# Kernel tuning notes

Measured on AMD Instinct MI355X. Metric: run time of the kernel, lower is better.

The kernel has to match this reference:

```python
import jax, jax.numpy as jnp
import numpy as np

NUM_HEADS = 16
D_MODEL = 2048
HEAD_DIM = 128
ROPE_BASE = 10000


def setup_inputs() -> dict:
    key = jax.random.key(0)
    k1, k2, k3 = jax.random.split(key, 3)
    B, S = 2, 2048
    x = jax.random.normal(k1, (B, S, D_MODEL), dtype=jnp.float32)
    attn_mask = jnp.ones((B, S), dtype=jnp.int32)
    in_proj = 0.02 * jax.random.normal(k2, (3, D_MODEL, NUM_HEADS, HEAD_DIM), dtype=jnp.float32)
    out_proj = 0.02 * jax.random.normal(k3, (NUM_HEADS, HEAD_DIM, D_MODEL), dtype=jnp.float32)
    return {"x": x, "attn_mask": attn_mask, "in_proj": in_proj, "out_proj": out_proj}


def _rope(t, seq_len):
    # t: [B, S, H, hd]; faithful to RotaryEmbedding.__call__ (concat layout, not interleaved)
    half = HEAD_DIM // 2
    inv_freq = 1.0 / (ROPE_BASE ** (2 * jnp.arange(0, half, dtype=jnp.float32) / HEAD_DIM))
    positions = jnp.arange(seq_len, dtype=jnp.float32)
    angles = positions[:, None] * inv_freq[None, :]            # [S, hd/2]
    cos = jnp.cos(angles)[None, :, None, :]                    # [1, S, 1, hd/2]
    sin = jnp.sin(angles)[None, :, None, :]
    tr = t.reshape(*t.shape[:-1], half, 2)                     # [B,S,H,hd/2,2]
    t0, t1 = tr[..., 0], tr[..., 1]
    out = jnp.concatenate([t0 * cos - t1 * sin, t0 * sin + t1 * cos], axis=-1)
    return out.reshape(t.shape)


def reference(x, attn_mask, in_proj, out_proj):
    B, S, D = x.shape
    qkv = jnp.einsum('bsd,tdhm->tbshm', x, in_proj)            # fused QKV
    q, k, v = qkv[0], qkv[1], qkv[2]
    q = _rope(q, S)
    k = _rope(k, S)
    q = jnp.einsum('bshd->bhsd', q)
    k = jnp.einsum('bshd->bhsd', k)
    v = jnp.einsum('bshd->bhsd', v)
    scores = jnp.einsum('bhqd,bhkd->bhqk', q, k) / jnp.sqrt(jnp.float32(HEAD_DIM))
    # causal mask * key padding mask, with diagonal forced to 1
    causal = jnp.tril(jnp.ones((S, S), dtype=scores.dtype))    # [S,S]
    key_mask = attn_mask.astype(scores.dtype)[:, None, :]      # [B,1,S]
    combined = causal[None, :, :] * key_mask                   # [B,S,S]
    eye = jnp.eye(S, dtype=bool)
    combined = jnp.where(eye[None, :, :], jnp.asarray(1.0, scores.dtype), combined)
    scores = scores + (-(1.0 - combined) * 1e9)[:, None, :, :]  # broadcast over heads
    attn_weights = jax.nn.softmax(scores, axis=-1)
    return jnp.einsum('bhqk,bhkd,hdo->bqo', attn_weights, v, out_proj)
```

## Files before the change

### kernel.cpp

```cpp
#include <hip/hip_runtime.h>
#include <hip/hip_bf16.h>

#define B_   2
#define S_   2048
#define H_   16
#define HD_  128
#define D_   2048
#define BS_  4096
#define SCALE_ 0.08838834764831845f

typedef __hip_bfloat16 bf16;
typedef float f32x4 __attribute__((ext_vector_type(4)));
typedef __bf16 bf16x8 __attribute__((ext_vector_type(8)));
typedef unsigned short u16x8 __attribute__((ext_vector_type(8)));
typedef unsigned short u16x4 __attribute__((ext_vector_type(4)));

static __device__ __forceinline__ unsigned short f2bf_u(float f) {
  bf16 h = __float2bfloat16(f);
  return __builtin_bit_cast(unsigned short, h);
}
static __device__ __forceinline__ void load_lds16(const void* g, void* l) {
  __builtin_amdgcn_global_load_lds((const __attribute__((address_space(1))) void*)g,
                                   (__attribute__((address_space(3))) void*)l, 16, 0, 0);
}

__global__ __launch_bounds__(256) void k_convert(const float* __restrict__ src,
                                                 bf16* __restrict__ dst) {
  const size_t i = ((size_t)blockIdx.x * 256 + threadIdx.x) * 8;
  const float4 a = *(const float4*)(src + i);
  const float4 b = *(const float4*)(src + i + 4);
  u16x8 o;
  o[0] = f2bf_u(a.x); o[1] = f2bf_u(a.y); o[2] = f2bf_u(a.z); o[3] = f2bf_u(a.w);
  o[4] = f2bf_u(b.x); o[5] = f2bf_u(b.y); o[6] = f2bf_u(b.z); o[7] = f2bf_u(b.w);
  *(u16x8*)(dst + i) = o;
}

__global__ __launch_bounds__(256) void k_transpose(const float* __restrict__ src0,
                                                   bf16* __restrict__ dst0) {
  const int z = blockIdx.z;
  const float* src = src0 + (size_t)z * D_ * D_;
  bf16* dst = dst0 + (size_t)z * D_ * D_;
  __shared__ float tile[64][65];
  const int t = threadIdx.x;
  const int x0 = blockIdx.x * 64, y0 = blockIdx.y * 64;
#pragma unroll
  for (int i = 0; i < 16; ++i) {
    int idx = t + i * 256, r = idx >> 6, c = idx & 63;
    tile[r][c] = src[(size_t)(y0 + r) * D_ + x0 + c];
  }
  __syncthreads();
#pragma unroll
  for (int i = 0; i < 16; ++i) {
    int idx = t + i * 256, c = idx >> 6, r = idx & 63;
    dst[(size_t)(x0 + c) * D_ + y0 + r] = __float2bfloat16(tile[r][c]);
  }
}

__global__ __launch_bounds__(256) void k_rope_tables(float* __restrict__ cost,
                                                     float* __restrict__ sint) {
  const int idx = blockIdx.x * 256 + threadIdx.x;
  const int s = idx >> 6, d = idx & 63;
  const float inv = expf(-(float)d * (9.210340371976184f / 64.f));
  const float ang = (float)s * inv;
  cost[idx] = cosf(ang);
  sint[idx] = sinf(ang);
}

template <int MODE>
__global__ __launch_bounds__(512, 4) void k_gemm_p(const bf16* __restrict__ A,
                                                   const bf16* __restrict__ Bt,
                                                   float* __restrict__ Cf,
                                                   bf16* __restrict__ qb,
                                                   bf16* __restrict__ kb,
                                                   bf16* __restrict__ vt,
                                                   const float* __restrict__ cost,
                                                   const float* __restrict__ sint) {
  extern __shared__ __align__(16) char smem[];
  const int tid = threadIdx.x;
  const int w = tid >> 6, lane = tid & 63;
  const int wm = w >> 2, wn = w & 3;
  const int lr = lane & 15, lg = lane >> 4;
  const int brow = blockIdx.x * 128, bcol = blockIdx.y * 256;

  f32x4 acc[4][4] = {};

  auto stage = [&](int kt, int buf) {
    char* base = smem + buf * 24576;
    {
      const int row = tid >> 2, su = tid & 3;
      const int up = su ^ ((row >> 1) & 3);
      load_lds16(A + (size_t)(brow + row) * D_ + kt * 32 + up * 8, base + w * 1024);
    }
#pragma unroll
    for (int i = 0; i < 2; ++i) {
      const int slot = i * 512 + tid;
      const int row = slot >> 2, su = slot & 3;
      const int up = su ^ ((row >> 1) & 3);
      load_lds16(Bt + (size_t)(bcol + row) * D_ + kt * 32 + up * 8,
                 base + 8192 + i * 8192 + w * 1024);
    }
  };

  const int NKT = D_ / 32;
  stage(0, 0); stage(1, 1);
  int bs = 0;
  for (int kt = 0; kt < NKT; ++kt) {
    if (kt < NKT - 1) asm volatile("s_waitcnt vmcnt(3)" ::: "memory");
    else              asm volatile("s_waitcnt vmcnt(0)" ::: "memory");
    __builtin_amdgcn_s_barrier();
    __builtin_amdgcn_sched_barrier(0);
    if (kt + 2 < NKT) {
      int sb = bs + 2; if (sb >= 3) sb -= 3;
      stage(kt + 2, sb);
    }

    const char* base = smem + bs * 24576;
    bf16x8 af[4], bf4[4];
#pragma unroll
    for (int q = 0; q < 4; ++q) {
      const int r = wm * 64 + q * 16 + lr;
      af[q] = *(const bf16x8*)(base + r * 64 + ((lg ^ ((r >> 1) & 3)) * 16));
    }
#pragma unroll
    for (int nf = 0; nf < 4; ++nf) {
      const int r = wn * 64 + nf * 16 + lr;
      bf4[nf] = *(const bf16x8*)(base + 8192 + r * 64 + ((lg ^ ((r >> 1) & 3)) * 16));
    }
    __builtin_amdgcn_s_setprio(1);
#pragma unroll
    for (int q = 0; q < 4; ++q)
#pragma unroll
      for (int nf = 0; nf < 4; ++nf)
        acc[q][nf] = __builtin_amdgcn_mfma_f32_16x16x32_bf16(af[q], bf4[nf], acc[q][nf], 0, 0, 0);
    __builtin_amdgcn_s_setprio(0);
    bs = (bs == 2) ? 0 : bs + 1;
  }

  if (MODE == 1) {
#pragma unroll
    for (int mf = 0; mf < 4; ++mf)
#pragma unroll
      for (int nf = 0; nf < 4; ++nf) {
        const int col = bcol + wn * 64 + nf * 16 + lr;
#pragma unroll
        for (int j = 0; j < 4; ++j) {
          const int row = brow + wm * 64 + mf * 16 + lg * 4 + j;
          Cf[(size_t)row * D_ + col] = acc[mf][nf][j];
        }
      }
  } else {
    const int t = bcol >> 11;
#pragma unroll
    for (int mf = 0; mf < 4; ++mf)
#pragma unroll
      for (int nf = 0; nf < 4; ++nf) {
        const int col = bcol + wn * 64 + nf * 16 + lr;
        const int h = (col >> 7) & (H_ - 1), mm = col & (HD_ - 1);
        if (t == 2) {
          const int row0 = brow + wm * 64 + mf * 16 + lg * 4;
          const int b = row0 >> 11, s0 = row0 & (S_ - 1);
          u16x4 pk;
#pragma unroll
          for (int j = 0; j < 4; ++j) pk[j] = f2bf_u(acc[mf][nf][j]);
          *(u16x4*)(vt + ((size_t)(b * H_ + h) * HD_ + mm) * S_ + s0) = pk;
        } else {
          const int i2 = mm >> 1;
          const bool odd = mm & 1;
#pragma unroll
          for (int j = 0; j < 4; ++j) {
            const int row = brow + wm * 64 + mf * 16 + lg * 4 + j;
            const int b = row >> 11, s = row & (S_ - 1);
            const float val = acc[mf][nf][j];
            const float part = __shfl_xor(val, 1, 64);
            const float c = cost[s * 64 + i2];
            const float sn = sint[s * 64 + i2];
            float o = odd ? (part * sn + val * c) : (val * c - part * sn);
            if (t == 0) o *= SCALE_;
            const int om = odd ? (64 + i2) : i2;
            bf16* dst = (t == 1) ? kb : qb;
            dst[((size_t)(b * H_ + h) * S_ + s) * HD_ + om] = __float2bfloat16(o);
          }
        }
      }
  }
}

__global__ __launch_bounds__(256, 2) void k_attn(const bf16* __restrict__ qb,
                                                 const bf16* __restrict__ kb,
                                                 const bf16* __restrict__ vt,
                                                 const int* __restrict__ mask,
                                                 bf16* __restrict__ attn_b) {
  const int tid = threadIdx.x, w = tid >> 6, lane = tid & 63;
  const int lr = lane & 15, lg = lane >> 4;
  const int qt = (blockIdx.y < 16) ? ((int)gridDim.x - 1 - (int)blockIdx.x)
                                   : (int)blockIdx.x;
  const int q0 = qt * 128;
  const int bh = blockIdx.y;
  const int b = bh >> 4, h = bh & (H_ - 1);
  const bf16* qp = qb + (size_t)bh * S_ * HD_;
  const bf16* kp = kb + (size_t)bh * S_ * HD_;
  const bf16* vp = vt + (size_t)bh * HD_ * S_;
  __shared__ __align__(16) bf16 Ks[2][64 * 128];
  __shared__ __align__(16) bf16 Vs[2][128 * 64];
  __shared__ __align__(16) bf16 Ps[4][16][80];

  const int qrowA = q0 + w * 16 + lr;
  bf16x8 qfA[4], qfB[4];
#pragma unroll
  for (int ks = 0; ks < 4; ++ks) {
    qfA[ks] = *(const bf16x8*)(qp + (size_t)qrowA * HD_ + ks * 32 + lg * 8);
    qfB[ks] = *(const bf16x8*)(qp + (size_t)(qrowA + 64) * HD_ + ks * 32 + lg * 8);
  }

  float mA[4], lA[4], mB[4], lB[4];
  f32x4 oA[8], oB[8];
#pragma unroll
  for (int j = 0; j < 4; ++j) { mA[j] = -INFINITY; lA[j] = 0.f; mB[j] = -INFINITY; lB[j] = 0.f; }
#pragma unroll
  for (int c = 0; c < 8; ++c) { oA[c] = (f32x4)(0.f); oB[c] = (f32x4)(0.f); }

  auto stage = [&](int buf, int k0) {
#pragma unroll
    for (int i = 0; i < 4; ++i) {
      const int slot = i * 256 + tid;
      const int row = slot >> 4, j16 = slot & 15;
      load_lds16(kp + (size_t)(k0 + row) * HD_ + ((j16 ^ (row & 7)) * 8),
                 (char*)&Ks[buf][0] + i * 4096 + w * 1024);
    }
#pragma unroll
    for (int i = 0; i < 4; ++i) {
      const int slot = i * 256 + tid;
      const int row = slot >> 3, j8 = slot & 7;
      load_lds16(vp + (size_t)row * S_ + k0 + ((j8 ^ (row & 7)) * 8),
                 (char*)&Vs[buf][0] + i * 4096 + w * 1024);
    }
  };

  auto sm_pv = [&](f32x4 (&sacc)[4], float (&m_run)[4], float (&l_run)[4],
                   f32x4 (&oacc)[8], const int rbase, const int k0,
                   const int (&mk4)[4], const bf16* vsb) {
    float mblk[4] = {-INFINITY, -INFINITY, -INFINITY, -INFINITY};
#pragma unroll
    for (int n = 0; n < 4; ++n) {
      const int kcol = k0 + n * 16 + lr;
#pragma unroll
      for (int j = 0; j < 4; ++j) {
        const int r = rbase + lg * 4 + j;
        float sv = sacc[n][j];
        const bool allowed = (kcol <= r) && (mk4[n] != 0 || kcol == r);
        sv = allowed ? sv : -1e9f;
        sacc[n][j] = sv;
        mblk[j] = fmaxf(mblk[j], sv);
      }
    }
#pragma unroll
    for (int xm = 1; xm < 16; xm <<= 1)
#pragma unroll
      for (int j = 0; j < 4; ++j)
        mblk[j] = fmaxf(mblk[j], __shfl_xor(mblk[j], xm, 64));

    bool grow = false;
#pragma unroll
    for (int j = 0; j < 4; ++j) grow = grow || (mblk[j] > m_run[j] + 8.f);
    if (__any(grow)) {
      float alpha[4];
#pragma unroll
      for (int j = 0; j < 4; ++j) {
        const float mn = fmaxf(m_run[j], mblk[j]);
        alpha[j] = __expf(m_run[j] - mn);
        m_run[j] = mn;
        l_run[j] *= alpha[j];
      }
#pragma unroll
      for (int c = 0; c < 8; ++c)
#pragma unroll
        for (int j = 0; j < 4; ++j) oacc[c][j] *= alpha[j];
    }

    float psum[4] = {0.f, 0.f, 0.f, 0.f};
#pragma unroll
    for (int n = 0; n < 4; ++n)
#pragma unroll
      for (int j = 0; j < 4; ++j) {
        const float p = __expf(sacc[n][j] - m_run[j]);
        psum[j] += p;
        sacc[n][j] = p;
      }
#pragma unroll
    for (int xm = 1; xm < 16; xm <<= 1)
#pragma unroll
      for (int j = 0; j < 4; ++j)
        psum[j] += __shfl_xor(psum[j], xm, 64);
#pragma unroll
    for (int j = 0; j < 4; ++j) l_run[j] += psum[j];

#pragma unroll
    for (int n = 0; n < 4; ++n)
#pragma unroll
      for (int j = 0; j < 4; ++j)
        Ps[w][lg * 4 + j][n * 16 + lr] = __float2bfloat16(sacc[n][j]);

    bf16x8 pa[2];
#pragma unroll
    for (int ks = 0; ks < 2; ++ks)
      pa[ks] = *(const bf16x8*)(&Ps[w][lr][ks * 32 + lg * 8]);
    __builtin_amdgcn_s_setprio(1);
#pragma unroll
    for (int c = 0; c < 8; ++c) {
#pragma unroll
      for (int ks = 0; ks < 2; ++ks) {
        const int vrow = c * 16 + lr;
        const int unit = (ks * 4 + lg) ^ (vrow & 7);
        const bf16x8 vf = *(const bf16x8*)(vsb + vrow * 64 + unit * 8);
        oacc[c] = __builtin_amdgcn_mfma_f32_16x16x32_bf16(pa[ks], vf, oacc[c], 0, 0, 0);
      }
    }
    __builtin_amdgcn_s_setprio(0);
  };

  const int nt = 2 * qt + 2;
  stage(0, 0);
  asm volatile("s_waitcnt vmcnt(0)" ::: "memory");
  __syncthreads();

  int cur = 0;
  for (int it = 0; it < nt; ++it) {
    const int k0 = it * 64;
    if (it + 1 < nt) stage(cur ^ 1, k0 + 64);

    int mk4[4];
#pragma unroll
    for (int n = 0; n < 4; ++n) mk4[n] = mask[b * S_ + k0 + n * 16 + lr];

    const bf16* ksb = &Ks[cur][0];
    const bf16* vsb = &Vs[cur][0];

    f32x4 sA[4] = {}, sB[4] = {};
    __builtin_amdgcn_s_setprio(1);
#pragma unroll
    for (int n = 0; n < 4; ++n) {
      const int krow = n * 16 + lr;
#pragma unroll
      for (int ks = 0; ks < 4; ++ks) {
        const int j16 = (ks * 4 + lg) ^ (krow & 7);
        const bf16x8 kf = *(const bf16x8*)(ksb + krow * 128 + j16 * 8);
        sA[n] = __builtin_amdgcn_mfma_f32_16x16x32_bf16(qfA[ks], kf, sA[n], 0, 0, 0);
        sB[n] = __builtin_amdgcn_mfma_f32_16x16x32_bf16(qfB[ks], kf, sB[n], 0, 0, 0);
      }
    }
    __builtin_amdgcn_s_setprio(0);

    sm_pv(sA, mA, lA, oA, q0 + w * 16, k0, mk4, vsb);
    sm_pv(sB, mB, lB, oB, q0 + 64 + w * 16, k0, mk4, vsb);

    asm volatile("s_waitcnt vmcnt(0)" ::: "memory");
    __syncthreads();
    cur ^= 1;
  }

#pragma unroll
  for (int j = 0; j < 4; ++j) {
    const float invA = 1.f / lA[j];
    const float invB = 1.f / lB[j];
    const int rA = q0 + w * 16 + lg * 4 + j;
#pragma unroll
    for (int c = 0; c < 8; ++c) {
      attn_b[(size_t)(b * S_ + rA) * D_ + h * HD_ + c * 16 + lr] =
          __float2bfloat16(oA[c][j] * invA);
      attn_b[(size_t)(b * S_ + rA + 64) * D_ + h * HD_ + c * 16 + lr] =
          __float2bfloat16(oB[c][j] * invB);
    }
  }
}

extern "C" void kernel_launch(void* const* d_in, const int* in_sizes, int n_in,
                              void* d_out, int out_size, void* d_ws, size_t ws_size,
                              hipStream_t stream) {
  (void)in_sizes; (void)n_in; (void)out_size; (void)ws_size;
  const float* x        = (const float*)d_in[0];
  const int*   attn_mask= (const int*)d_in[1];
  const float* in_proj  = (const float*)d_in[2];
  const float* out_proj = (const float*)d_in[3];
  float* out = (float*)d_out;
  char* ws = (char*)d_ws;

  bf16*  xb    = (bf16*)(ws + 0);
  bf16*  wqkvT = (bf16*)(ws + 16777216);
  bf16*  woT   = (bf16*)(ws + 41943040);
  float* cost  = (float*)(ws + 50331648);
  float* sint  = (float*)(ws + 50855936);
  bf16*  vt    = (bf16*)(ws + 51380224);
  bf16* qb = (bf16*)d_out;
  bf16* kb = (bf16*)((char*)d_out + 16777216);
  bf16* attn_b = xb;

  static int lds_ok = 0;
  if (!lds_ok) {
    (void)hipFuncSetAttribute((const void*)k_gemm_p<0>,
                              hipFuncAttributeMaxDynamicSharedMemorySize, 73728);
    (void)hipFuncSetAttribute((const void*)k_gemm_p<1>,
                              hipFuncAttributeMaxDynamicSharedMemorySize, 73728);
    lds_ok = 1;
  }

  k_convert<<<4096, 256, 0, stream>>>(x, xb);
  k_transpose<<<dim3(32, 32, 3), 256, 0, stream>>>(in_proj, wqkvT);
  k_transpose<<<dim3(32, 32, 1), 256, 0, stream>>>(out_proj, woT);
  k_rope_tables<<<512, 256, 0, stream>>>(cost, sint);
  k_gemm_p<0><<<dim3(32, 24), 512, 73728, stream>>>(xb, wqkvT, nullptr, qb, kb, vt, cost, sint);
  k_attn<<<dim3(16, 32), 256, 0, stream>>>(qb, kb, vt, attn_mask, attn_b);
  k_gemm_p<1><<<dim3(32, 8), 512, 73728, stream>>>(attn_b, woT, out, nullptr, nullptr, nullptr,
                                                   nullptr, nullptr);
}
```

Before: 302.5 us.

## Read V fragments from global memory, share them across row halves, skip masked last tile

```diff
diff --git a/kernel.cpp b/kernel.cpp
--- a/kernel.cpp
+++ b/kernel.cpp
@@ -201,8 +201,7 @@
   const bf16* kp = kb + (size_t)bh * S_ * HD_;
   const bf16* vp = vt + (size_t)bh * HD_ * S_;
   __shared__ __align__(16) bf16 Ks[2][64 * 128];
-  __shared__ __align__(16) bf16 Vs[2][128 * 64];
-  __shared__ __align__(16) bf16 Ps[4][16][80];
+  __shared__ __align__(16) bf16 Ps[4][2][16][80];
 
   const int qrowA = q0 + w * 16 + lr;
   bf16x8 qfA[4], qfB[4];
@@ -219,7 +218,7 @@
 #pragma unroll
   for (int c = 0; c < 8; ++c) { oA[c] = (f32x4)(0.f); oB[c] = (f32x4)(0.f); }
 
-  auto stage = [&](int buf, int k0) {
+  auto stageK = [&](int buf, int k0) {
 #pragma unroll
     for (int i = 0; i < 4; ++i) {
       const int slot = i * 256 + tid;
@@ -227,18 +226,11 @@
       load_lds16(kp + (size_t)(k0 + row) * HD_ + ((j16 ^ (row & 7)) * 8),
                  (char*)&Ks[buf][0] + i * 4096 + w * 1024);
     }
-#pragma unroll
-    for (int i = 0; i < 4; ++i) {
-      const int slot = i * 256 + tid;
-      const int row = slot >> 3, j8 = slot & 7;
-      load_lds16(vp + (size_t)row * S_ + k0 + ((j8 ^ (row & 7)) * 8),
-                 (char*)&Vs[buf][0] + i * 4096 + w * 1024);
-    }
   };
 
-  auto sm_pv = [&](f32x4 (&sacc)[4], float (&m_run)[4], float (&l_run)[4],
-                   f32x4 (&oacc)[8], const int rbase, const int k0,
-                   const int (&mk4)[4], const bf16* vsb) {
+  auto softmax_g = [&](f32x4 (&sacc)[4], float (&m_run)[4], float (&l_run)[4],
+                       f32x4 (&oacc)[8], const int rbase, const int k0,
+                       const int (&mk4)[4], const int g, bf16x8 (&pa)[2]) {
     float mblk[4] = {-INFINITY, -INFINITY, -INFINITY, -INFINITY};
 #pragma unroll
     for (int n = 0; n < 4; ++n) {
@@ -298,42 +290,28 @@
     for (int n = 0; n < 4; ++n)
 #pragma unroll
       for (int j = 0; j < 4; ++j)
-        Ps[w][lg * 4 + j][n * 16 + lr] = __float2bfloat16(sacc[n][j]);
-
-    bf16x8 pa[2];
+        Ps[w][g][lg * 4 + j][n * 16 + lr] = __float2bfloat16(sacc[n][j]);
 #pragma unroll
     for (int ks = 0; ks < 2; ++ks)
-      pa[ks] = *(const bf16x8*)(&Ps[w][lr][ks * 32 + lg * 8]);
-    __builtin_amdgcn_s_setprio(1);
-#pragma unroll
-    for (int c = 0; c < 8; ++c) {
-#pragma unroll
-      for (int ks = 0; ks < 2; ++ks) {
-        const int vrow = c * 16 + lr;
-        const int unit = (ks * 4 + lg) ^ (vrow & 7);
-        const bf16x8 vf = *(const bf16x8*)(vsb + vrow * 64 + unit * 8);
-        oacc[c] = __builtin_amdgcn_mfma_f32_16x16x32_bf16(pa[ks], vf, oacc[c], 0, 0, 0);
-      }
-    }
-    __builtin_amdgcn_s_setprio(0);
+      pa[ks] = *(const bf16x8*)(&Ps[w][g][lr][ks * 32 + lg * 8]);
   };
 
   const int nt = 2 * qt + 2;
-  stage(0, 0);
+  stageK(0, 0);
   asm volatile("s_waitcnt vmcnt(0)" ::: "memory");
   __syncthreads();
 
   int cur = 0;
   for (int it = 0; it < nt; ++it) {
     const int k0 = it * 64;
-    if (it + 1 < nt) stage(cur ^ 1, k0 + 64);
+    const bool doA = (it + 1 < nt);
+    if (it + 1 < nt) stageK(cur ^ 1, k0 + 64);
 
     int mk4[4];
 #pragma unroll
     for (int n = 0; n < 4; ++n) mk4[n] = mask[b * S_ + k0 + n * 16 + lr];
 
     const bf16* ksb = &Ks[cur][0];
-    const bf16* vsb = &Vs[cur][0];
 
     f32x4 sA[4] = {}, sB[4] = {};
     __builtin_amdgcn_s_setprio(1);
@@ -344,14 +322,27 @@
       for (int ks = 0; ks < 4; ++ks) {
         const int j16 = (ks * 4 + lg) ^ (krow & 7);
         const bf16x8 kf = *(const bf16x8*)(ksb + krow * 128 + j16 * 8);
-        sA[n] = __builtin_amdgcn_mfma_f32_16x16x32_bf16(qfA[ks], kf, sA[n], 0, 0, 0);
+        if (doA) sA[n] = __builtin_amdgcn_mfma_f32_16x16x32_bf16(qfA[ks], kf, sA[n], 0, 0, 0);
         sB[n] = __builtin_amdgcn_mfma_f32_16x16x32_bf16(qfB[ks], kf, sB[n], 0, 0, 0);
       }
     }
     __builtin_amdgcn_s_setprio(0);
 
-    sm_pv(sA, mA, lA, oA, q0 + w * 16, k0, mk4, vsb);
-    sm_pv(sB, mB, lB, oB, q0 + 64 + w * 16, k0, mk4, vsb);
+    bf16x8 paA[2], paB[2];
+    if (doA) softmax_g(sA, mA, lA, oA, q0 + w * 16, k0, mk4, 0, paA);
+    softmax_g(sB, mB, lB, oB, q0 + 64 + w * 16, k0, mk4, 1, paB);
+
+    __builtin_amdgcn_s_setprio(1);
+#pragma unroll
+    for (int c = 0; c < 8; ++c) {
+#pragma unroll
+      for (int ks = 0; ks < 2; ++ks) {
+        const bf16x8 vf = *(const bf16x8*)(vp + (size_t)(c * 16 + lr) * S_ + k0 + ks * 32 + lg * 8);
+        if (doA) oA[c] = __builtin_amdgcn_mfma_f32_16x16x32_bf16(paA[ks], vf, oA[c], 0, 0, 0);
+        oB[c] = __builtin_amdgcn_mfma_f32_16x16x32_bf16(paB[ks], vf, oB[c], 0, 0, 0);
+      }
+    }
+    __builtin_amdgcn_s_setprio(0);
 
     asm volatile("s_waitcnt vmcnt(0)" ::: "memory");
     __syncthreads();
```

Result: slower. 404.9 us (+33.8%).
